# Performance work log

Measured on AMD Instinct MI355X. Metric: run time of the kernel, lower is better.

The kernel has to match this reference:

```python
import jax, jax.numpy as jnp
import numpy as np

T, B = 2048, 32
LIS, SPE, ATT = 1024, 1024, 512


def setup_inputs() -> dict:
    key = jax.random.key(0)
    ks = jax.random.split(key, 10)
    s = 0.02
    return {
        "listener_state": jax.random.normal(ks[0], (T, B, LIS), jnp.float32),
        "speller_state": jax.random.normal(ks[1], (B, SPE), jnp.float32),
        "listener_len": jax.random.randint(ks[2], (B,), 1, T + 1),
        "batch_size": B,
        "W_score": jax.random.normal(ks[3], (LIS, ATT), jnp.float32) * s,
        "b_score": jnp.zeros((ATT,), jnp.float32),
        "W_value": jax.random.normal(ks[4], (LIS, ATT), jnp.float32) * s,
        "b_value": jnp.zeros((ATT,), jnp.float32),
        "W_proj": jax.random.normal(ks[5], (SPE, ATT), jnp.float32) * s,
        "b_proj": jnp.zeros((ATT,), jnp.float32),
    }


def reference(listener_state, speller_state, listener_len, batch_size,
              W_score, b_score, W_value, b_value, W_proj, b_proj):
    # batch_first=False path: [T,B,D] -> [B,T,D]
    x = jnp.transpose(listener_state, (1, 0, 2))
    keys = jax.nn.relu(x @ W_score + b_score)          # [B,T,A]
    vals = jax.nn.relu(x @ W_value + b_value)          # [B,T,A]
    query = jax.nn.relu(speller_state @ W_proj + b_proj)  # [B,A]
    scores = jnp.einsum('ba,bta->bt', query, keys)     # [B,T]
    # vectorized length mask: additive -100 past valid length (faithful to source)
    t = jnp.arange(keys.shape[1])
    mask = jnp.where(t[None, :] >= listener_len[:, None], -100.0, 0.0)
    attn = jax.nn.softmax(scores + mask, axis=1)       # [B,T]
    context = jnp.einsum('bt,bta->ba', attn, vals)     # [B,A]
    return (context, attn)
```

## Files before the change

### kernel.cpp

```cpp
#include <hip/hip_runtime.h>
#include <hip/hip_bf16.h>
#include <hip/hip_fp16.h>

#define T_DIM 2048
#define B_DIM 32
#define LIS_DIM 1024
#define SPE_DIM 1024
#define ATT_DIM 512

typedef _Float16 f16x8 __attribute__((ext_vector_type(8)));
typedef _Float16 f16x4 __attribute__((ext_vector_type(4)));
typedef float f32x4 __attribute__((ext_vector_type(4)));

__global__ void transpose_w_kernel(const float* __restrict__ Ws,
                                   const float* __restrict__ Wv,
                                   _Float16* __restrict__ WTf) {
  __shared__ float t17[1024 * 17];
  int blk = blockIdx.x;
  int mat = blk >> 5, ct = blk & 31;
  int tid = threadIdx.x;
  const float* W = mat ? Wv : Ws;
  for (int e = tid; e < 16384; e += 256) {
    int k = e >> 4, c = e & 15;
    t17[k * 17 + c] = W[(size_t)k * ATT_DIM + ct * 16 + c];
  }
  __syncthreads();
  int wv4 = tid >> 6, lane = tid & 63, lo = lane & 15, hi = lane >> 4;
  for (int ks = wv4; ks < 32; ks += 4) {
    f16x8 h;
#pragma unroll
    for (int j = 0; j < 8; ++j)
      h[j] = (_Float16)t17[(ks * 32 + hi * 8 + j) * 17 + lo];
    ((f16x8*)WTf)[((size_t)((mat * 32 + ct) * 32 + ks)) * 64 + lane] = h;
  }
}

__global__ void query_kernel(const float* __restrict__ spe,
                             const float* __restrict__ Wp,
                             const float* __restrict__ bp,
                             float* __restrict__ q) {
  __shared__ float s[SPE_DIM];
  int b = blockIdx.x;
  for (int i = threadIdx.x; i < SPE_DIM; i += 256) s[i] = spe[(size_t)b * SPE_DIM + i];
  __syncthreads();
  for (int a = threadIdx.x; a < ATT_DIM; a += 256) {
    float acc = bp[a];
    for (int l = 0; l < SPE_DIM; ++l)
      acc = fmaf(s[l], Wp[(size_t)l * ATT_DIM + a], acc);
    q[(size_t)b * ATT_DIM + a] = fmaxf(acc, 0.f);
  }
}

__global__ __launch_bounds__(512)
void dual_gemm_kernel(const float* __restrict__ x,
                      const _Float16* __restrict__ WTf,
                      const float* __restrict__ bs,
                      const float* __restrict__ bv,
                      const float* __restrict__ q,
                      float* __restrict__ scores,
                      _Float16* __restrict__ vals_p) {
  __shared__ __align__(16) char A_lds[2][16384];
  __shared__ float bk_s[ATT_DIM], bv_s[ATT_DIM], q_s[ATT_DIM];
  __shared__ float red_s[64];

  const int tid = threadIdx.x;
  const int blk = blockIdx.x;
  const int b = blk & 31;
  const int tc = blk >> 5;
  const int t0 = tc * 64;

  bk_s[tid] = bs[tid];
  bv_s[tid] = bv[tid];
  q_s[tid] = q[(size_t)b * ATT_DIM + tid];
  if (tid < 64) red_s[tid] = 0.f;

  const float* xb = x + (size_t)b * LIS_DIM;
  const int wv = tid >> 6;
  const int lane = tid & 63;
  const int lo = lane & 15;
  const int hi = lane >> 4;

  auto stage = [&](int c, char* buf) {
    const int k0 = c * 128;
#pragma unroll
    for (int it = 0; it < 4; ++it) {
      int idx = it * 512 + tid;
      int row = idx >> 5;
      int c4 = idx & 31;
      const float4 f =
          ((const float4*)(xb + (size_t)(t0 + row) * (B_DIM * LIS_DIM) + k0))[c4];
      f16x4 h;
      h[0] = (_Float16)f.x; h[1] = (_Float16)f.y;
      h[2] = (_Float16)f.z; h[3] = (_Float16)f.w;
      int off = (row * 256 + c4 * 8) ^ ((row & 7) << 4);
      *(f16x4*)(buf + off) = h;
    }
  };

  f32x4 kacc[4][4], vacc[4][4];
#pragma unroll
  for (int m = 0; m < 4; ++m)
#pragma unroll
    for (int n = 0; n < 4; ++n) {
      kacc[m][n] = (f32x4){0.f, 0.f, 0.f, 0.f};
      vacc[m][n] = (f32x4){0.f, 0.f, 0.f, 0.f};
    }

  stage(0, A_lds[0]);
  __syncthreads();

  const f16x8* Wf = (const f16x8*)WTf;

  for (int c = 0; c < 8; ++c) {
    if (c < 7) stage(c + 1, A_lds[(c + 1) & 1]);
    const char* buf = A_lds[c & 1];
#pragma unroll
    for (int kki = 0; kki < 4; ++kki) {
      const int kk = kki * 32;
      const int ks = c * 4 + kki;
      f16x8 bx[4];
#pragma unroll
      for (int m = 0; m < 4; ++m) {
        int row = m * 16 + lo;
        int off = (row * 256 + kk * 2 + hi * 16) ^ ((row & 7) << 4);
        bx[m] = *(const f16x8*)(buf + off);
      }
#pragma unroll
      for (int n = 0; n < 4; ++n) {
        int ct = wv * 4 + n;
        f16x8 wk  = Wf[(size_t)(ct * 32 + ks) * 64 + lane];
        f16x8 wvv = Wf[(size_t)((32 + ct) * 32 + ks) * 64 + lane];
#pragma unroll
        for (int m = 0; m < 4; ++m) {
          kacc[m][n] = __builtin_amdgcn_mfma_f32_16x16x32_f16(wk,  bx[m], kacc[m][n], 0, 0, 0);
          vacc[m][n] = __builtin_amdgcn_mfma_f32_16x16x32_f16(wvv, bx[m], vacc[m][n], 0, 0, 0);
        }
      }
    }
    __syncthreads();
  }

  _Float16* vp = vals_p + ((size_t)(b * 32 + tc) * 8 + wv) * 4096;
#pragma unroll
  for (int m = 0; m < 4; ++m)
#pragma unroll
    for (int n = 0; n < 4; ++n) {
      int col = wv * 64 + n * 16 + hi * 4;
      f16x4 h;
#pragma unroll
      for (int r = 0; r < 4; ++r)
        h[r] = (_Float16)fmaxf(vacc[m][n][r] + bv_s[col + r], 0.f);
      *(f16x4*)(vp + (m * 4 + n) * 256 + lane * 4) = h;
    }

  float sr[4] = {0.f, 0.f, 0.f, 0.f};
#pragma unroll
  for (int m = 0; m < 4; ++m)
#pragma unroll
    for (int n = 0; n < 4; ++n) {
      int col = wv * 64 + n * 16 + hi * 4;
#pragma unroll
      for (int r = 0; r < 4; ++r)
        sr[m] += q_s[col + r] * fmaxf(kacc[m][n][r] + bk_s[col + r], 0.f);
    }
#pragma unroll
  for (int m = 0; m < 4; ++m) {
    sr[m] += __shfl_xor(sr[m], 16, 64);
    sr[m] += __shfl_xor(sr[m], 32, 64);
    if (lane < 16) atomicAdd(&red_s[m * 16 + lo], sr[m]);
  }
  __syncthreads();
  if (tid < 64) scores[(size_t)b * T_DIM + t0 + tid] = red_s[tid];
}

__global__ void softmax_kernel(const float* __restrict__ scores,
                               const int* __restrict__ llen,
                               float* __restrict__ attn_out,
                               float* __restrict__ ctx_out) {
  __shared__ float rmax[4], rsum[4];
  int b = blockIdx.x, tid = threadIdx.x;
  int L = llen[b];
  float v[8];
  float mx = -1e30f;
  for (int i = 0; i < 8; ++i) {
    int t = i * 256 + tid;
    float s = scores[(size_t)b * T_DIM + t];
    if (t >= L) s -= 100.f;
    v[i] = s;
    mx = fmaxf(mx, s);
  }
  for (int d = 1; d < 64; d <<= 1) mx = fmaxf(mx, __shfl_xor(mx, d, 64));
  if ((tid & 63) == 0) rmax[tid >> 6] = mx;
  __syncthreads();
  mx = fmaxf(fmaxf(rmax[0], rmax[1]), fmaxf(rmax[2], rmax[3]));
  float sum = 0.f;
  for (int i = 0; i < 8; ++i) { v[i] = expf(v[i] - mx); sum += v[i]; }
  for (int d = 1; d < 64; d <<= 1) sum += __shfl_xor(sum, d, 64);
  if ((tid & 63) == 0) rsum[tid >> 6] = sum;
  __syncthreads();
  sum = rsum[0] + rsum[1] + rsum[2] + rsum[3];
  float inv = 1.f / sum;
  for (int i = 0; i < 8; ++i) {
    int t = i * 256 + tid;
    attn_out[(size_t)b * T_DIM + t] = v[i] * inv;
  }
  for (int i = tid; i < ATT_DIM; i += 256) ctx_out[(size_t)b * ATT_DIM + i] = 0.f;
}

__global__ __launch_bounds__(512)
void ctx_kernel(const _Float16* __restrict__ vals_p,
                const float* __restrict__ attn,
                float* __restrict__ ctx) {
  __shared__ float attn_s[512];
  int blk = blockIdx.x;
  int b = blk >> 2, tcg = blk & 3;
  int tid = threadIdx.x;
  int wv = tid >> 6, lane = tid & 63, lo = lane & 15, hi = lane >> 4;
  attn_s[tid] = attn[(size_t)b * T_DIM + tcg * 512 + tid];
  __syncthreads();
  float cacc[4][4] = {};
  for (int i = 0; i < 8; ++i) {
    int tc = tcg * 8 + i;
    const _Float16* vp = vals_p + ((size_t)(b * 32 + tc) * 8 + wv) * 4096;
#pragma unroll
    for (int m = 0; m < 4; ++m) {
      float w = attn_s[i * 64 + m * 16 + lo];
#pragma unroll
      for (int n = 0; n < 4; ++n) {
        f16x4 v = *(const f16x4*)(vp + (m * 4 + n) * 256 + lane * 4);
#pragma unroll
        for (int r = 0; r < 4; ++r) cacc[n][r] += w * (float)v[r];
      }
    }
  }
#pragma unroll
  for (int n = 0; n < 4; ++n)
#pragma unroll
    for (int r = 0; r < 4; ++r) {
      float v = cacc[n][r];
      v += __shfl_xor(v, 1, 64);
      v += __shfl_xor(v, 2, 64);
      v += __shfl_xor(v, 4, 64);
      v += __shfl_xor(v, 8, 64);
      if (lo == 0)
        atomicAdd(&ctx[(size_t)b * ATT_DIM + wv * 64 + n * 16 + hi * 4 + r], v);
    }
}

extern "C" void kernel_launch(void* const* d_in, const int* in_sizes, int n_in,
                              void* d_out, int out_size, void* d_ws, size_t ws_size,
                              hipStream_t stream) {
  const float* x   = (const float*)d_in[0];
  const float* spe = (const float*)d_in[1];
  const int*   len = (const int*)d_in[2];
  const float* Ws  = (const float*)d_in[4];
  const float* bs  = (const float*)d_in[5];
  const float* Wv  = (const float*)d_in[6];
  const float* bv  = (const float*)d_in[7];
  const float* Wp  = (const float*)d_in[8];
  const float* bp  = (const float*)d_in[9];
  float* out = (float*)d_out;

  char* ws = (char*)d_ws;
  _Float16* WTf  = (_Float16*)ws;
  float* q       = (float*)(ws + (2u << 20));
  float* scores  = (float*)(ws + (2u << 20) + (64u << 10));
  _Float16* vals = (_Float16*)(ws + (4u << 20));

  transpose_w_kernel<<<dim3(64), dim3(256), 0, stream>>>(Ws, Wv, WTf);
  query_kernel<<<dim3(32), dim3(256), 0, stream>>>(spe, Wp, bp, q);
  dual_gemm_kernel<<<dim3(1024), dim3(512), 0, stream>>>(x, WTf, bs, bv, q, scores, vals);
  softmax_kernel<<<dim3(32), dim3(256), 0, stream>>>(scores, len, out + 16384, out);
  ctx_kernel<<<dim3(128), dim3(512), 0, stream>>>(vals, out + 16384, out);
}
```

Before: 299.4 us.

## Split activation staging into load/write phases and double-buffer weight fragments

Activation staging is split so the global fp32 loads for the next K chunk are issued before the MFMA loop and their fp16 conversion and LDS write happen after it, hiding global latency behind compute. Weight fragments for the next k-step are prefetched into a two-slot register buffer while the current MFMAs run. Launch bounds now request two blocks per CU. The extra live registers (float4 staging plus doubled weight fragments) under the tighter occupancy bound risk spills.

```diff
diff --git a/kernel.cpp b/kernel.cpp
--- a/kernel.cpp
+++ b/kernel.cpp
@@ -51,7 +51,7 @@
   }
 }
 
-__global__ __launch_bounds__(512)
+__global__ __launch_bounds__(512, 2)
 void dual_gemm_kernel(const float* __restrict__ x,
                       const _Float16* __restrict__ WTf,
                       const float* __restrict__ bs,
@@ -80,18 +80,27 @@
   const int lo = lane & 15;
   const int hi = lane >> 4;
 
-  auto stage = [&](int c, char* buf) {
+  float4 sl[4];
+  auto stage_load = [&](int c) {
     const int k0 = c * 128;
 #pragma unroll
     for (int it = 0; it < 4; ++it) {
       int idx = it * 512 + tid;
       int row = idx >> 5;
       int c4 = idx & 31;
-      const float4 f =
-          ((const float4*)(xb + (size_t)(t0 + row) * (B_DIM * LIS_DIM) + k0))[c4];
+      sl[it] = ((const float4*)(xb + (size_t)(t0 + row) * (B_DIM * LIS_DIM) + k0))[c4];
+    }
+  };
+  auto stage_write = [&](int c) {
+    char* buf = A_lds[c & 1];
+#pragma unroll
+    for (int it = 0; it < 4; ++it) {
+      int idx = it * 512 + tid;
+      int row = idx >> 5;
+      int c4 = idx & 31;
       f16x4 h;
-      h[0] = (_Float16)f.x; h[1] = (_Float16)f.y;
-      h[2] = (_Float16)f.z; h[3] = (_Float16)f.w;
+      h[0] = (_Float16)sl[it].x; h[1] = (_Float16)sl[it].y;
+      h[2] = (_Float16)sl[it].z; h[3] = (_Float16)sl[it].w;
       int off = (row * 256 + c4 * 8) ^ ((row & 7) << 4);
       *(f16x4*)(buf + off) = h;
     }
@@ -106,37 +115,47 @@
       vacc[m][n] = (f32x4){0.f, 0.f, 0.f, 0.f};
     }
 
-  stage(0, A_lds[0]);
+  stage_load(0);
+  stage_write(0);
   __syncthreads();
 
   const f16x8* Wf = (const f16x8*)WTf;
+  f16x8 wkf[2][4], wvf[2][4];
+#pragma unroll
+  for (int n = 0; n < 4; ++n) {
+    wkf[0][n] = Wf[(size_t)((wv * 4 + n) * 32 + 0) * 64 + lane];
+    wvf[0][n] = Wf[(size_t)((32 + wv * 4 + n) * 32 + 0) * 64 + lane];
+  }
 
   for (int c = 0; c < 8; ++c) {
-    if (c < 7) stage(c + 1, A_lds[(c + 1) & 1]);
+    if (c < 7) stage_load(c + 1);
     const char* buf = A_lds[c & 1];
 #pragma unroll
     for (int kki = 0; kki < 4; ++kki) {
-      const int kk = kki * 32;
       const int ks = c * 4 + kki;
+      const int kp = (ks + 1 < 32) ? ks + 1 : 31;
+      const int cur = kki & 1, nxt = cur ^ 1;
+#pragma unroll
+      for (int n = 0; n < 4; ++n) {
+        wkf[nxt][n] = Wf[(size_t)((wv * 4 + n) * 32 + kp) * 64 + lane];
+        wvf[nxt][n] = Wf[(size_t)((32 + wv * 4 + n) * 32 + kp) * 64 + lane];
+      }
       f16x8 bx[4];
 #pragma unroll
       for (int m = 0; m < 4; ++m) {
         int row = m * 16 + lo;
-        int off = (row * 256 + kk * 2 + hi * 16) ^ ((row & 7) << 4);
+        int off = (row * 256 + kki * 64 + hi * 16) ^ ((row & 7) << 4);
         bx[m] = *(const f16x8*)(buf + off);
       }
 #pragma unroll
-      for (int n = 0; n < 4; ++n) {
-        int ct = wv * 4 + n;
-        f16x8 wk  = Wf[(size_t)(ct * 32 + ks) * 64 + lane];
-        f16x8 wvv = Wf[(size_t)((32 + ct) * 32 + ks) * 64 + lane];
+      for (int n = 0; n < 4; ++n)
 #pragma unroll
         for (int m = 0; m < 4; ++m) {
-          kacc[m][n] = __builtin_amdgcn_mfma_f32_16x16x32_f16(wk,  bx[m], kacc[m][n], 0, 0, 0);
-          vacc[m][n] = __builtin_amdgcn_mfma_f32_16x16x32_f16(wvv, bx[m], vacc[m][n], 0, 0, 0);
+          kacc[m][n] = __builtin_amdgcn_mfma_f32_16x16x32_f16(wkf[cur][n], bx[m], kacc[m][n], 0, 0, 0);
+          vacc[m][n] = __builtin_amdgcn_mfma_f32_16x16x32_f16(wvf[cur][n], bx[m], vacc[m][n], 0, 0, 0);
         }
-      }
-    }
+    }
+    if (c < 7) stage_write(c + 1);
     __syncthreads();
   }
 
```

Result: slower. 308.9 us (+3.2%).
